# Kernel tuning notes

Measured on AMD Instinct MI355X. Metric: run time of the kernel, lower is better.

## Reference

```python
import jax, jax.numpy as jnp
import numpy as np

N, NFEAT, NHID, NCLASS = 16384, 512, 64, 40
K, ALPHA = 10, 0.1


def setup_inputs() -> dict:
    key = jax.random.key(0)
    k1, k2, k3, k4 = jax.random.split(key, 4)
    x = jax.random.normal(k1, (N, NFEAT), dtype=jnp.float32)
    # dense (row-normalized) propagation matrix, as a PPR transition matrix
    adj = jax.random.uniform(k2, (N, N), dtype=jnp.float32)
    adj = adj / jnp.sum(adj, axis=1, keepdims=True)
    # kaiming-like scaled weights (bias=False in the module)
    W1 = jax.random.normal(k3, (NFEAT, NHID), dtype=jnp.float32) * np.sqrt(2.0 / NFEAT)
    W2 = jax.random.normal(k4, (NHID, NCLASS), dtype=jnp.float32) * np.sqrt(2.0 / NHID)
    return {"x": x, "adj": adj, "W1": W1, "W2": W2}


def reference(x, adj, W1, W2):
    # eval mode: dropout is identity
    h0 = jax.nn.relu(x @ W1)                      # [N, NHID]
    # K-step personalized-PageRank propagation
    def step(x_cl, _):
        return (1.0 - ALPHA) * (adj @ x_cl) + ALPHA * h0, None
    x_cl, _ = jax.lax.scan(step, h0, None, length=K)
    h = x_cl @ W2                                 # [N, NCLASS]
    return jax.nn.log_softmax(h, axis=-1), x_cl
```

## Files before the change

### kernel.cpp

```cpp
#include <hip/hip_runtime.h>

#define NN 16384
#define NF 512
#define NH 64
#define NC 40
#define KSTEPS 10
#define KSPLIT 8
#define BM 32
#define PKH 8
#define ASCALE 8192.0f

typedef __attribute__((ext_vector_type(8))) short short8;
typedef __attribute__((ext_vector_type(4))) float f32x4;
typedef __attribute__((ext_vector_type(2))) long longx2;

__device__ __forceinline__ unsigned short f2bf(float f) {
    unsigned int u = __float_as_uint(f);
    u += 0x7FFFu + ((u >> 16) & 1u);
    return (unsigned short)(u >> 16);
}
__device__ __forceinline__ float bf2f(unsigned short h) {
    return __uint_as_float((unsigned int)h << 16);
}
__device__ __forceinline__ short8 cvt8(float4 f0, float4 f1) {
    short8 r;
    r[0] = (short)f2bf(f0.x); r[1] = (short)f2bf(f0.y);
    r[2] = (short)f2bf(f0.z); r[3] = (short)f2bf(f0.w);
    r[4] = (short)f2bf(f1.x); r[5] = (short)f2bf(f1.y);
    r[6] = (short)f2bf(f1.z); r[7] = (short)f2bf(f1.w);
    return r;
}
__device__ __forceinline__ int pack4fp8(float x0, float x1, float x2, float x3) {
    int r = __builtin_amdgcn_cvt_pk_fp8_f32(x0, x1, 0, false);
    return __builtin_amdgcn_cvt_pk_fp8_f32(x2, x3, r, true);
}
__device__ __forceinline__ longx2 ntload_l2(const unsigned char* p) {
    return __builtin_nontemporal_load((const longx2*)p);
}

__global__ __launch_bounds__(256) void h0_kernel(const float* __restrict__ x,
                                                 const float* __restrict__ W1,
                                                 unsigned short* __restrict__ h0T) {
    const int t  = threadIdx.x;
    const int rl = t & 63;
    const int w  = t >> 6;
    const size_t r = (size_t)blockIdx.x * 64 + rl;
    const float* xr = x + r * NF;

    float acc[16];
#pragma unroll
    for (int j = 0; j < 16; ++j) acc[j] = 0.f;

    for (int k = 0; k < NF; k += 4) {
        float4 xv = *(const float4*)&xr[k];
#pragma unroll
        for (int i = 0; i < 4; ++i) {
            float xs = (i == 0) ? xv.x : (i == 1) ? xv.y : (i == 2) ? xv.z : xv.w;
            const float* wr = W1 + (size_t)(k + i) * NH + w * 16;
#pragma unroll
            for (int j = 0; j < 16; ++j) acc[j] = fmaf(xs, wr[j], acc[j]);
        }
    }
#pragma unroll
    for (int j = 0; j < 16; ++j)
        h0T[(size_t)(w * 16 + j) * NN + r] = f2bf(fmaxf(acc[j], 0.f));
}

__global__ __launch_bounds__(256) void cvtfp8_kernel(const unsigned short* __restrict__ in,
                                                     unsigned char* __restrict__ out,
                                                     long n8) {
    long i = (long)blockIdx.x * blockDim.x + threadIdx.x;
    if (i >= n8) return;
    short8 v = *(const short8*)&in[i * 8];
    int2 o;
    o.x = pack4fp8(bf2f((unsigned short)v[0]), bf2f((unsigned short)v[1]),
                   bf2f((unsigned short)v[2]), bf2f((unsigned short)v[3]));
    o.y = pack4fp8(bf2f((unsigned short)v[4]), bf2f((unsigned short)v[5]),
                   bf2f((unsigned short)v[6]), bf2f((unsigned short)v[7]));
    *(int2*)&out[i * 8] = o;
}

__device__ __forceinline__ void finish_block(float buf[KSPLIT][BM][65],
                                             const f32x4 (&acc)[2][4],
                                             int t, int l, int w, int row0,
                                             const unsigned short* __restrict__ h0T,
                                             unsigned short* __restrict__ xnT,
                                             unsigned char* __restrict__ xnT8) {
    const int fr = l & 15;
    const int fg = l >> 4;
#pragma unroll
    for (int mi = 0; mi < 2; ++mi)
#pragma unroll
        for (int ni = 0; ni < 4; ++ni)
#pragma unroll
            for (int r = 0; r < 4; ++r)
                buf[w][16 * mi + 4 * fg + r][16 * ni + fr] = acc[mi][ni][r];
    __syncthreads();

    const int col = t >> 3;
    const int rb  = 4 * (t & 7);
    float s0 = 0.f, s1 = 0.f, s2 = 0.f, s3 = 0.f;
#pragma unroll
    for (int ww = 0; ww < KSPLIT; ++ww) {
        s0 += buf[ww][rb + 0][col];
        s1 += buf[ww][rb + 1][col];
        s2 += buf[ww][rb + 2][col];
        s3 += buf[ww][rb + 3][col];
    }
    const size_t base = (size_t)col * NN + row0 + rb;
    ushort4 h4 = *(const ushort4*)&h0T[base];
    float v0 = 0.9f * s0 + 0.1f * bf2f(h4.x);
    float v1 = 0.9f * s1 + 0.1f * bf2f(h4.y);
    float v2 = 0.9f * s2 + 0.1f * bf2f(h4.z);
    float v3 = 0.9f * s3 + 0.1f * bf2f(h4.w);
    ushort4 o;
    o.x = f2bf(v0); o.y = f2bf(v1); o.z = f2bf(v2); o.w = f2bf(v3);
    *(ushort4*)&xnT[base] = o;
    if (xnT8)
        *(int*)&xnT8[base] = pack4fp8(v0, v1, v2, v3);
}

__global__ __launch_bounds__(512, 2) void step0_kernel(
        const float* __restrict__ adj,
        unsigned char* __restrict__ adjT8,
        const unsigned short* __restrict__ xT,
        const unsigned short* __restrict__ h0T,
        unsigned short* __restrict__ xnT,
        unsigned char* __restrict__ xnT8) {
    __shared__ float buf[KSPLIT][BM][65];

    const int t    = threadIdx.x;
    const int l    = t & 63;
    const int w    = t >> 6;
    const int fr   = l & 15;
    const int fg   = l >> 4;
    const int row0 = blockIdx.x * BM;

    const size_t a0 = (size_t)(row0 + fr) * NN;
    const size_t a1 = a0 + (size_t)16 * NN;
    const long   kbase = (long)w * (NN / KSPLIT) + 8 * fg;

    f32x4 acc[2][4];
#pragma unroll
    for (int mi = 0; mi < 2; ++mi)
#pragma unroll
        for (int ni = 0; ni < 4; ++ni) acc[mi][ni] = (f32x4){0.f, 0.f, 0.f, 0.f};

    for (int kk = 0; kk < NN / KSPLIT; kk += 64) {
        const long kb      = kbase + kk;
        const size_t ktile = (size_t)w * 32 + (kk >> 6);
        short8 a[2][2], b[4][2];

#pragma unroll
        for (int mi = 0; mi < 2; ++mi) {
            const size_t ab = (mi ? a1 : a0);
            int4 pk;
#pragma unroll
            for (int h = 0; h < 2; ++h) {
                float4 f0 = *(const float4*)&adj[ab + kb + 32 * h];
                float4 f1 = *(const float4*)&adj[ab + kb + 32 * h + 4];
                a[mi][h] = cvt8(f0, f1);
                int plo = pack4fp8(ASCALE * f0.x, ASCALE * f0.y,
                                   ASCALE * f0.z, ASCALE * f0.w);
                int phi = pack4fp8(ASCALE * f1.x, ASCALE * f1.y,
                                   ASCALE * f1.z, ASCALE * f1.w);
                if (h == 0) { pk.x = plo; pk.y = phi; }
                else        { pk.z = plo; pk.w = phi; }
            }
            const size_t st = ((size_t)(2 * blockIdx.x + mi) * 256 + ktile) * 1024
                              + (size_t)l * 16;
            *(int4*)&adjT8[st] = pk;
        }
#pragma unroll
        for (int ni = 0; ni < 4; ++ni)
#pragma unroll
            for (int h = 0; h < 2; ++h)
                b[ni][h] = *(const short8*)&xT[(size_t)(16 * ni + fr) * NN + kb + 32 * h];

#pragma unroll
        for (int mi = 0; mi < 2; ++mi)
#pragma unroll
            for (int ni = 0; ni < 4; ++ni)
#pragma unroll
                for (int h = 0; h < 2; ++h)
                    acc[mi][ni] = __builtin_amdgcn_mfma_f32_16x16x32_bf16(
                        a[mi][h], b[ni][h], acc[mi][ni], 0, 0, 0);
    }
    finish_block(buf, acc, t, l, w, row0, h0T, xnT, xnT8);
}

__global__ __launch_bounds__(512, 4) void stept_kernel(
        const unsigned char* __restrict__ adjT8,
        const unsigned char* __restrict__ xT8,
        float* __restrict__ P) {
    __shared__ unsigned char BLF[2][4096];

    const int t  = threadIdx.x;
    const int l  = t & 63;
    const int w  = t >> 6;
    const int fr = l & 15;
    const int fg = l >> 4;
    const int kh = blockIdx.x & 7;
    const int rt = blockIdx.x >> 3;
    const int kb0 = kh * (NN / PKH);

    const unsigned char* At0 = adjT8
        + (((size_t)(rt * 16 + 2 * w) * 256) + (size_t)(kh * 32)) * 1024 + (size_t)l * 16;
    const unsigned char* At1 = At0 + (size_t)256 * 1024;

    const size_t bsrc = (size_t)(16 * (w >> 1) + fr) * NN + 32 * (w & 1) + 8 * fg;
    unsigned char* st0 = &BLF[0][t * 8];
    unsigned char* st1 = &BLF[1][t * 8];

    f32x4 acc[2][4];
#pragma unroll
    for (int mi = 0; mi < 2; ++mi)
#pragma unroll
        for (int ni = 0; ni < 4; ++ni) acc[mi][ni] = (f32x4){0.f, 0.f, 0.f, 0.f};

    *(long*)st0 = *(const long*)&xT8[bsrc + kb0];
    __syncthreads();

#pragma unroll 2
    for (int i = 0; i < 32; ++i) {
        const unsigned char* rdbuf = (i & 1) ? BLF[1] : BLF[0];
        unsigned char* stbuf = (i & 1) ? st0 : st1;
        if (i + 1 < 32)
            *(long*)stbuf = *(const long*)&xT8[bsrc + kb0 + (i + 1) * 64];

        longx2 a0 = ntload_l2(At0);
        longx2 a1 = ntload_l2(At1);
        At0 += 1024;
        At1 += 1024;

        long b[4][2];
#pragma unroll
        for (int ni = 0; ni < 4; ++ni)
#pragma unroll
            for (int h = 0; h < 2; ++h)
                b[ni][h] = *(const long*)&rdbuf[(size_t)((ni * 2 + h) * 64 + l) * 8];

#pragma unroll
        for (int ni = 0; ni < 4; ++ni) {
            acc[0][ni] = __builtin_amdgcn_mfma_f32_16x16x32_fp8_fp8(a0.x, b[ni][0], acc[0][ni], 0, 0, 0);
            acc[0][ni] = __builtin_amdgcn_mfma_f32_16x16x32_fp8_fp8(a0.y, b[ni][1], acc[0][ni], 0, 0, 0);
            acc[1][ni] = __builtin_amdgcn_mfma_f32_16x16x32_fp8_fp8(a1.x, b[ni][0], acc[1][ni], 0, 0, 0);
            acc[1][ni] = __builtin_amdgcn_mfma_f32_16x16x32_fp8_fp8(a1.y, b[ni][1], acc[1][ni], 0, 0, 0);
        }
        __syncthreads();
    }

    const size_t rowbase = (size_t)rt * 256 + w * 32;
#pragma unroll
    for (int mi = 0; mi < 2; ++mi)
#pragma unroll
        for (int ni = 0; ni < 4; ++ni)
#pragma unroll
            for (int r = 0; r < 4; ++r)
                P[(((size_t)kh * NN) + rowbase + mi * 16 + 4 * fg + r) * 64 + 16 * ni + fr]
                    = acc[mi][ni][r];
}

__global__ __launch_bounds__(256) void combine_kernel(
        const float* __restrict__ P,
        const unsigned short* __restrict__ h0T,
        unsigned short* __restrict__ xnT,
        unsigned char* __restrict__ xnT8) {
    __shared__ float LS[64][65];
    const int t  = threadIdx.x;
    const int r0 = blockIdx.x * 64;

    {
        const int rl = t >> 2;
        const int c0 = (t & 3) * 16;
        f32x4 s[4];
#pragma unroll
        for (int q = 0; q < 4; ++q) s[q] = (f32x4){0.f, 0.f, 0.f, 0.f};
#pragma unroll
        for (int kh = 0; kh < PKH; ++kh) {
            const float* p = &P[(((size_t)kh * NN) + r0 + rl) * 64 + c0];
#pragma unroll
            for (int q = 0; q < 4; ++q) s[q] += *(const f32x4*)&p[q * 4];
        }
#pragma unroll
        for (int q = 0; q < 4; ++q)
            *(f32x4*)&LS[rl][c0 + q * 4] = s[q];
    }
    __syncthreads();

    {
        const int c  = t >> 2;
        const int rs = (t & 3) * 16;
        float vf[16];
        short8 v[2];
#pragma unroll
        for (int j = 0; j < 16; ++j) {
            vf[j] = (0.9f / ASCALE) * LS[rs + j][c]
                  + 0.1f * bf2f(h0T[(size_t)c * NN + r0 + rs + j]);
            v[j >> 3][j & 7] = (short)f2bf(vf[j]);
        }
        *(short8*)&xnT[(size_t)c * NN + r0 + rs]     = v[0];
        *(short8*)&xnT[(size_t)c * NN + r0 + rs + 8] = v[1];
        int4 pk;
        pk.x = pack4fp8(vf[0],  vf[1],  vf[2],  vf[3]);
        pk.y = pack4fp8(vf[4],  vf[5],  vf[6],  vf[7]);
        pk.z = pack4fp8(vf[8],  vf[9],  vf[10], vf[11]);
        pk.w = pack4fp8(vf[12], vf[13], vf[14], vf[15]);
        *(int4*)&xnT8[(size_t)c * NN + r0 + rs] = pk;
    }
}

__global__ __launch_bounds__(512, 4) void stepf_kernel(
        const float* __restrict__ adj,
        const unsigned short* __restrict__ xT,
        const unsigned short* __restrict__ h0T,
        unsigned short* __restrict__ xnT) {
    __shared__ float buf[KSPLIT][BM][65];

    const int t    = threadIdx.x;
    const int l    = t & 63;
    const int w    = t >> 6;
    const int fr   = l & 15;
    const int row0 = blockIdx.x * BM;

    const size_t a0 = (size_t)(row0 + fr) * NN;
    const size_t a1 = a0 + (size_t)16 * NN;
    const long   kbase = (long)w * (NN / KSPLIT) + 8 * (l >> 4);

    f32x4 acc[2][4];
#pragma unroll
    for (int mi = 0; mi < 2; ++mi)
#pragma unroll
        for (int ni = 0; ni < 4; ++ni) acc[mi][ni] = (f32x4){0.f, 0.f, 0.f, 0.f};

    for (int kk = 0; kk < NN / KSPLIT; kk += 64) {
        const long kb = kbase + kk;
        short8 a[2][2], b[4][2];
#pragma unroll
        for (int mi = 0; mi < 2; ++mi) {
            const size_t ab = (mi ? a1 : a0);
#pragma unroll
            for (int h = 0; h < 2; ++h) {
                float4 f0 = *(const float4*)&adj[ab + kb + 32 * h];
                float4 f1 = *(const float4*)&adj[ab + kb + 32 * h + 4];
                a[mi][h] = cvt8(f0, f1);
            }
        }
#pragma unroll
        for (int ni = 0; ni < 4; ++ni)
#pragma unroll
            for (int h = 0; h < 2; ++h)
                b[ni][h] = *(const short8*)&xT[(size_t)(16 * ni + fr) * NN + kb + 32 * h];
#pragma unroll
        for (int mi = 0; mi < 2; ++mi)
#pragma unroll
            for (int ni = 0; ni < 4; ++ni)
#pragma unroll
                for (int h = 0; h < 2; ++h)
                    acc[mi][ni] = __builtin_amdgcn_mfma_f32_16x16x32_bf16(
                        a[mi][h], b[ni][h], acc[mi][ni], 0, 0, 0);
    }
    finish_block(buf, acc, t, l, w, row0, h0T, xnT, nullptr);
}

__global__ __launch_bounds__(256) void final_kernel(const unsigned short* __restrict__ xT,
                                                    const float* __restrict__ W2,
                                                    float* __restrict__ out_ls,
                                                    float* __restrict__ out_x) {
    __shared__ float LS[64][65];
    const int t  = threadIdx.x;
    const int rl = t & 63;
    const int w  = t >> 6;
    const int r0 = blockIdx.x * 64;

#pragma unroll
    for (int j = 0; j < 16; ++j) {
        int c = w * 16 + j;
        LS[c][rl] = bf2f(xT[(size_t)c * NN + r0 + rl]);
    }
    __syncthreads();

#pragma unroll
    for (int k2 = 0; k2 < 16; ++k2) {
        int idx = k2 * 256 + t;
        int row = idx >> 6, col = idx & 63;
        out_x[(size_t)(r0 + row) * NH + col] = LS[col][row];
    }

    float acc[NC];
    if (t < 64) {
#pragma unroll
        for (int j = 0; j < NC; ++j) acc[j] = 0.f;
        for (int c = 0; c < NH; ++c) {
            float xv = LS[c][t];
            const float* wr = W2 + (size_t)c * NC;
#pragma unroll
            for (int j = 0; j < NC; ++j) acc[j] = fmaf(xv, wr[j], acc[j]);
        }
        float m = acc[0];
#pragma unroll
        for (int j = 1; j < NC; ++j) m = fmaxf(m, acc[j]);
        float s = 0.f;
#pragma unroll
        for (int j = 0; j < NC; ++j) s += expf(acc[j] - m);
        float lg = m + logf(s);
#pragma unroll
        for (int j = 0; j < NC; ++j) acc[j] -= lg;
    }
    __syncthreads();
    if (t < 64) {
#pragma unroll
        for (int j = 0; j < NC; ++j) LS[t][j] = acc[j];
    }
    __syncthreads();
    for (int i = t; i < 64 * NC; i += 256) {
        int row = i / NC, j = i - row * NC;
        out_ls[(size_t)r0 * NC + i] = LS[row][j];
    }
}

extern "C" void kernel_launch(void* const* d_in, const int* in_sizes, int n_in,
                              void* d_out, int out_size, void* d_ws, size_t ws_size,
                              hipStream_t stream) {
    const float* x   = (const float*)d_in[0];
    const float* adj = (const float*)d_in[1];
    const float* W1  = (const float*)d_in[2];
    const float* W2  = (const float*)d_in[3];

    float* out_ls = (float*)d_out;
    float* out_x  = out_ls + (size_t)NN * NC;

    const size_t xbytes  = (size_t)NN * NH * sizeof(unsigned short);
    const size_t x8bytes = (size_t)NN * NH;
    char* ws = (char*)d_ws;

    unsigned short *h0T, *xa, *xb;
    unsigned char  *h0T8, *xa8, *xb8;
    size_t used;
    if (ws_size >= 3 * xbytes + 3 * x8bytes) {
        h0T  = (unsigned short*)ws;
        xa   = (unsigned short*)(ws + xbytes);
        xb   = (unsigned short*)(ws + 2 * xbytes);
        h0T8 = (unsigned char*)(ws + 3 * xbytes);
        xa8  = h0T8 + x8bytes;
        xb8  = xa8 + x8bytes;
        used = 3 * xbytes + 3 * x8bytes;
    } else {
        xa  = (unsigned short*)ws;
        xb  = xa + (size_t)NN * NH;
        h0T = (unsigned short*)out_ls;
        h0T8 = xa8 = xb8 = nullptr;
        used = 2 * xbytes;
    }
    used = (used + 255) & ~(size_t)255;

    const size_t pbytes    = (size_t)PKH * NN * NH * sizeof(float);
    const size_t adj8bytes = (size_t)NN * NN;

    float* P = nullptr;
    unsigned char* adjT8 = nullptr;
    if (h0T8 && ws_size >= used + pbytes + adj8bytes) {
        P     = (float*)(ws + used);
        adjT8 = (unsigned char*)(ws + used + pbytes);
    }

    h0_kernel<<<NN / 64, 256, 0, stream>>>(x, W1, h0T);

    unsigned short* cur  = h0T;
    unsigned short* nxt  = xa;
    unsigned char*  cur8 = h0T8;
    unsigned char*  nxt8 = xa8;

    if (adjT8)
        cvtfp8_kernel<<<(NN * NH / 8 + 255) / 256, 256, 0, stream>>>(
            h0T, h0T8, (long)NN * NH / 8);

    for (int s = 0; s < KSTEPS; ++s) {
        if (adjT8) {
            if (s == 0) {
                step0_kernel<<<NN / BM, 512, 0, stream>>>(adj, adjT8, cur, h0T, nxt, nxt8);
            } else {
                stept_kernel<<<(NN / 256) * PKH, 512, 0, stream>>>(adjT8, cur8, P);
                combine_kernel<<<NN / 64, 256, 0, stream>>>(P, h0T, nxt, nxt8);
            }
        } else {
            stepf_kernel<<<NN / BM, 512, 0, stream>>>(adj, cur, h0T, nxt);
        }
        unsigned short* ts  = (cur == h0T) ? xb : cur;
        unsigned char*  ts8 = (cur8 == h0T8) ? xb8 : cur8;
        cur = nxt;  nxt = ts;
        cur8 = nxt8; nxt8 = ts8;
    }

    final_kernel<<<NN / 64, 256, 0, stream>>>(cur, W2, out_ls, out_x);
}
```

Before: 1.048 ms.

## Restructure step0 into split-K tiles via LDS, store partials as bf16

The first propagation step is rewritten to use 16-row tiles split eight ways along K, like the later fp8 steps. Each block stages the fp32 adjacency rows into LDS as bf16, then packs them into the transposed fp8 layout. Partial sums go to a shared buffer reduced by combine_kernel, which now takes a scale argument. The partial buffer P drops from fp32 to bf16 to halve its write and read traffic. The separate h0 fp8 conversion kernel is removed, at the cost of extra bf16 rounding in the partials.

```diff
diff --git a/kernel.cpp b/kernel.cpp
--- a/kernel.cpp
+++ b/kernel.cpp
@@ -66,133 +66,108 @@
         h0T[(size_t)(w * 16 + j) * NN + r] = f2bf(fmaxf(acc[j], 0.f));
 }
 
-__global__ __launch_bounds__(256) void cvtfp8_kernel(const unsigned short* __restrict__ in,
-                                                     unsigned char* __restrict__ out,
-                                                     long n8) {
-    long i = (long)blockIdx.x * blockDim.x + threadIdx.x;
-    if (i >= n8) return;
-    short8 v = *(const short8*)&in[i * 8];
-    int2 o;
-    o.x = pack4fp8(bf2f((unsigned short)v[0]), bf2f((unsigned short)v[1]),
-                   bf2f((unsigned short)v[2]), bf2f((unsigned short)v[3]));
-    o.y = pack4fp8(bf2f((unsigned short)v[4]), bf2f((unsigned short)v[5]),
-                   bf2f((unsigned short)v[6]), bf2f((unsigned short)v[7]));
-    *(int2*)&out[i * 8] = o;
-}
-
-__device__ __forceinline__ void finish_block(float buf[KSPLIT][BM][65],
-                                             const f32x4 (&acc)[2][4],
-                                             int t, int l, int w, int row0,
-                                             const unsigned short* __restrict__ h0T,
-                                             unsigned short* __restrict__ xnT,
-                                             unsigned char* __restrict__ xnT8) {
-    const int fr = l & 15;
-    const int fg = l >> 4;
-#pragma unroll
-    for (int mi = 0; mi < 2; ++mi)
-#pragma unroll
-        for (int ni = 0; ni < 4; ++ni)
-#pragma unroll
-            for (int r = 0; r < 4; ++r)
-                buf[w][16 * mi + 4 * fg + r][16 * ni + fr] = acc[mi][ni][r];
-    __syncthreads();
-
-    const int col = t >> 3;
-    const int rb  = 4 * (t & 7);
-    float s0 = 0.f, s1 = 0.f, s2 = 0.f, s3 = 0.f;
-#pragma unroll
-    for (int ww = 0; ww < KSPLIT; ++ww) {
-        s0 += buf[ww][rb + 0][col];
-        s1 += buf[ww][rb + 1][col];
-        s2 += buf[ww][rb + 2][col];
-        s3 += buf[ww][rb + 3][col];
-    }
-    const size_t base = (size_t)col * NN + row0 + rb;
-    ushort4 h4 = *(const ushort4*)&h0T[base];
-    float v0 = 0.9f * s0 + 0.1f * bf2f(h4.x);
-    float v1 = 0.9f * s1 + 0.1f * bf2f(h4.y);
-    float v2 = 0.9f * s2 + 0.1f * bf2f(h4.z);
-    float v3 = 0.9f * s3 + 0.1f * bf2f(h4.w);
-    ushort4 o;
-    o.x = f2bf(v0); o.y = f2bf(v1); o.z = f2bf(v2); o.w = f2bf(v3);
-    *(ushort4*)&xnT[base] = o;
-    if (xnT8)
-        *(int*)&xnT8[base] = pack4fp8(v0, v1, v2, v3);
-}
-
-__global__ __launch_bounds__(512, 2) void step0_kernel(
+__global__ __launch_bounds__(512, 4) void step0_kernel(
         const float* __restrict__ adj,
         unsigned char* __restrict__ adjT8,
         const unsigned short* __restrict__ xT,
-        const unsigned short* __restrict__ h0T,
-        unsigned short* __restrict__ xnT,
-        unsigned char* __restrict__ xnT8) {
-    __shared__ float buf[KSPLIT][BM][65];
-
-    const int t    = threadIdx.x;
-    const int l    = t & 63;
-    const int w    = t >> 6;
-    const int fr   = l & 15;
-    const int fg   = l >> 4;
-    const int row0 = blockIdx.x * BM;
-
-    const size_t a0 = (size_t)(row0 + fr) * NN;
-    const size_t a1 = a0 + (size_t)16 * NN;
-    const long   kbase = (long)w * (NN / KSPLIT) + 8 * fg;
-
-    f32x4 acc[2][4];
-#pragma unroll
-    for (int mi = 0; mi < 2; ++mi)
-#pragma unroll
-        for (int ni = 0; ni < 4; ++ni) acc[mi][ni] = (f32x4){0.f, 0.f, 0.f, 0.f};
-
-    for (int kk = 0; kk < NN / KSPLIT; kk += 64) {
-        const long kb      = kbase + kk;
-        const size_t ktile = (size_t)w * 32 + (kk >> 6);
-        short8 a[2][2], b[4][2];
-
-#pragma unroll
-        for (int mi = 0; mi < 2; ++mi) {
-            const size_t ab = (mi ? a1 : a0);
+        unsigned short* __restrict__ P) {
+    __shared__ __align__(16) unsigned char SMEM[33280];
+    unsigned short (*AT)[1032] = (unsigned short (*)[1032])SMEM;
+    float (*FB)[16][65] = (float (*)[16][65])SMEM;
+
+    const int t  = threadIdx.x;
+    const int l  = t & 63;
+    const int w  = t >> 6;
+    const int fr = l & 15;
+    const int fg = l >> 4;
+    const int kh = blockIdx.x & 7;
+    const int mt = blockIdx.x >> 3;
+    const int r0 = mt * 16;
+    const long ks0 = (long)kh * (NN / PKH);
+
+    f32x4 acc[4];
+#pragma unroll
+    for (int ni = 0; ni < 4; ++ni) acc[ni] = (f32x4){0.f, 0.f, 0.f, 0.f};
+
+#pragma unroll
+    for (int chunk = 0; chunk < 2; ++chunk) {
+        const long kc0 = ks0 + chunk * 1024;
+        __syncthreads();
+#pragma unroll
+        for (int rr = 0; rr < 2; ++rr) {
+            const int row = 2 * w + rr;
+            const float* src = &adj[(size_t)(r0 + row) * NN + kc0];
+#pragma unroll
+            for (int q = 0; q < 4; ++q) {
+                float4 v = *(const float4*)&src[q * 256 + l * 4];
+                ushort4 o;
+                o.x = f2bf(v.x); o.y = f2bf(v.y); o.z = f2bf(v.z); o.w = f2bf(v.w);
+                *(ushort4*)&AT[row][q * 256 + l * 4] = o;
+            }
+        }
+        __syncthreads();
+#pragma unroll
+        for (int tt = 0; tt < 2; ++tt) {
+            const int tl = 2 * w + tt;
+            short8 a0 = *(const short8*)&AT[fr][tl * 64 + 8 * fg];
+            short8 a1 = *(const short8*)&AT[fr][tl * 64 + 32 + 8 * fg];
+
             int4 pk;
-#pragma unroll
-            for (int h = 0; h < 2; ++h) {
-                float4 f0 = *(const float4*)&adj[ab + kb + 32 * h];
-                float4 f1 = *(const float4*)&adj[ab + kb + 32 * h + 4];
-                a[mi][h] = cvt8(f0, f1);
-                int plo = pack4fp8(ASCALE * f0.x, ASCALE * f0.y,
-                                   ASCALE * f0.z, ASCALE * f0.w);
-                int phi = pack4fp8(ASCALE * f1.x, ASCALE * f1.y,
-                                   ASCALE * f1.z, ASCALE * f1.w);
-                if (h == 0) { pk.x = plo; pk.y = phi; }
-                else        { pk.z = plo; pk.w = phi; }
-            }
-            const size_t st = ((size_t)(2 * blockIdx.x + mi) * 256 + ktile) * 1024
+            pk.x = pack4fp8(ASCALE * bf2f((unsigned short)a0[0]),
+                            ASCALE * bf2f((unsigned short)a0[1]),
+                            ASCALE * bf2f((unsigned short)a0[2]),
+                            ASCALE * bf2f((unsigned short)a0[3]));
+            pk.y = pack4fp8(ASCALE * bf2f((unsigned short)a0[4]),
+                            ASCALE * bf2f((unsigned short)a0[5]),
+                            ASCALE * bf2f((unsigned short)a0[6]),
+                            ASCALE * bf2f((unsigned short)a0[7]));
+            pk.z = pack4fp8(ASCALE * bf2f((unsigned short)a1[0]),
+                            ASCALE * bf2f((unsigned short)a1[1]),
+                            ASCALE * bf2f((unsigned short)a1[2]),
+                            ASCALE * bf2f((unsigned short)a1[3]));
+            pk.w = pack4fp8(ASCALE * bf2f((unsigned short)a1[4]),
+                            ASCALE * bf2f((unsigned short)a1[5]),
+                            ASCALE * bf2f((unsigned short)a1[6]),
+                            ASCALE * bf2f((unsigned short)a1[7]));
+            const size_t st = ((size_t)mt * 256 + kh * 32 + chunk * 16 + tl) * 1024
                               + (size_t)l * 16;
             *(int4*)&adjT8[st] = pk;
-        }
-#pragma unroll
-        for (int ni = 0; ni < 4; ++ni)
-#pragma unroll
-            for (int h = 0; h < 2; ++h)
-                b[ni][h] = *(const short8*)&xT[(size_t)(16 * ni + fr) * NN + kb + 32 * h];
-
-#pragma unroll
-        for (int mi = 0; mi < 2; ++mi)
-#pragma unroll
-            for (int ni = 0; ni < 4; ++ni)
-#pragma unroll
-                for (int h = 0; h < 2; ++h)
-                    acc[mi][ni] = __builtin_amdgcn_mfma_f32_16x16x32_bf16(
-                        a[mi][h], b[ni][h], acc[mi][ni], 0, 0, 0);
-    }
-    finish_block(buf, acc, t, l, w, row0, h0T, xnT, xnT8);
+
+            const long kb = kc0 + tl * 64 + 8 * fg;
+#pragma unroll
+            for (int ni = 0; ni < 4; ++ni) {
+                short8 b0 = *(const short8*)&xT[(size_t)(16 * ni + fr) * NN + kb];
+                short8 b1 = *(const short8*)&xT[(size_t)(16 * ni + fr) * NN + kb + 32];
+                acc[ni] = __builtin_amdgcn_mfma_f32_16x16x32_bf16(a0, b0, acc[ni], 0, 0, 0);
+                acc[ni] = __builtin_amdgcn_mfma_f32_16x16x32_bf16(a1, b1, acc[ni], 0, 0, 0);
+            }
+        }
+    }
+
+    __syncthreads();
+#pragma unroll
+    for (int ni = 0; ni < 4; ++ni)
+#pragma unroll
+        for (int r = 0; r < 4; ++r)
+            FB[w][4 * fg + r][16 * ni + fr] = acc[ni][r];
+    __syncthreads();
+
+    const int col = t & 63;
+    const int rw2 = t >> 6;
+#pragma unroll
+    for (int rr = 0; rr < 2; ++rr) {
+        const int row = 2 * rw2 + rr;
+        float s = 0.f;
+#pragma unroll
+        for (int ww = 0; ww < 8; ++ww) s += FB[ww][row][col];
+        P[((size_t)kh * NN + r0 + row) * 64 + col] = f2bf(s);
+    }
 }
 
 __global__ __launch_bounds__(512, 4) void stept_kernel(
         const unsigned char* __restrict__ adjT8,
         const unsigned char* __restrict__ xT8,
-        float* __restrict__ P) {
+        unsigned short* __restrict__ P) {
     __shared__ unsigned char BLF[2][4096];
 
     const int t  = threadIdx.x;
@@ -258,14 +233,15 @@
 #pragma unroll
             for (int r = 0; r < 4; ++r)
                 P[(((size_t)kh * NN) + rowbase + mi * 16 + 4 * fg + r) * 64 + 16 * ni + fr]
-                    = acc[mi][ni][r];
+                    = f2bf(acc[mi][ni][r]);
 }
 
 __global__ __launch_bounds__(256) void combine_kernel(
-        const float* __restrict__ P,
+        const unsigned short* __restrict__ P,
         const unsigned short* __restrict__ h0T,
         unsigned short* __restrict__ xnT,
-        unsigned char* __restrict__ xnT8) {
+        unsigned char* __restrict__ xnT8,
+        float scale) {
     __shared__ float LS[64][65];
     const int t  = threadIdx.x;
     const int r0 = blockIdx.x * 64;
@@ -273,18 +249,22 @@
     {
         const int rl = t >> 2;
         const int c0 = (t & 3) * 16;
-        f32x4 s[4];
-#pragma unroll
-        for (int q = 0; q < 4; ++q) s[q] = (f32x4){0.f, 0.f, 0.f, 0.f};
+        float s[16];
+#pragma unroll
+        for (int j = 0; j < 16; ++j) s[j] = 0.f;
 #pragma unroll
         for (int kh = 0; kh < PKH; ++kh) {
-            const float* p = &P[(((size_t)kh * NN) + r0 + rl) * 64 + c0];
-#pragma unroll
-            for (int q = 0; q < 4; ++q) s[q] += *(const f32x4*)&p[q * 4];
-        }
-#pragma unroll
-        for (int q = 0; q < 4; ++q)
-            *(f32x4*)&LS[rl][c0 + q * 4] = s[q];
+            const unsigned short* p = &P[(((size_t)kh * NN) + r0 + rl) * 64 + c0];
+            short8 v0 = *(const short8*)&p[0];
+            short8 v1 = *(const short8*)&p[8];
+#pragma unroll
+            for (int j = 0; j < 8; ++j) {
+                s[j]     += bf2f((unsigned short)v0[j]);
+                s[8 + j] += bf2f((unsigned short)v1[j]);
+            }
+        }
+#pragma unroll
+        for (int j = 0; j < 16; ++j) LS[rl][c0 + j] = s[j];
     }
     __syncthreads();
 
@@ -295,7 +275,7 @@
         short8 v[2];
 #pragma unroll
         for (int j = 0; j < 16; ++j) {
-            vf[j] = (0.9f / ASCALE) * LS[rs + j][c]
+            vf[j] = scale * LS[rs + j][c]
                   + 0.1f * bf2f(h0T[(size_t)c * NN + r0 + rs + j]);
             v[j >> 3][j & 7] = (short)f2bf(vf[j]);
         }
@@ -310,6 +290,42 @@
     }
 }
 
+__device__ __forceinline__ void finish_blockf(float buf[KSPLIT][BM][65],
+                                              const f32x4 (&acc)[2][4],
+                                              int t, int l, int w, int row0,
+                                              const unsigned short* __restrict__ h0T,
+                                              unsigned short* __restrict__ xnT) {
+    const int fr = l & 15;
+    const int fg = l >> 4;
+#pragma unroll
+    for (int mi = 0; mi < 2; ++mi)
+#pragma unroll
+        for (int ni = 0; ni < 4; ++ni)
+#pragma unroll
+            for (int r = 0; r < 4; ++r)
+                buf[w][16 * mi + 4 * fg + r][16 * ni + fr] = acc[mi][ni][r];
+    __syncthreads();
+
+    const int col = t >> 3;
+    const int rb  = 4 * (t & 7);
+    float s0 = 0.f, s1 = 0.f, s2 = 0.f, s3 = 0.f;
+#pragma unroll
+    for (int ww = 0; ww < KSPLIT; ++ww) {
+        s0 += buf[ww][rb + 0][col];
+        s1 += buf[ww][rb + 1][col];
+        s2 += buf[ww][rb + 2][col];
+        s3 += buf[ww][rb + 3][col];
+    }
+    const size_t base = (size_t)col * NN + row0 + rb;
+    ushort4 h4 = *(const ushort4*)&h0T[base];
+    ushort4 o;
+    o.x = f2bf(0.9f * s0 + 0.1f * bf2f(h4.x));
+    o.y = f2bf(0.9f * s1 + 0.1f * bf2f(h4.y));
+    o.z = f2bf(0.9f * s2 + 0.1f * bf2f(h4.z));
+    o.w = f2bf(0.9f * s3 + 0.1f * bf2f(h4.w));
+    *(ushort4*)&xnT[base] = o;
+}
+
 __global__ __launch_bounds__(512, 4) void stepf_kernel(
         const float* __restrict__ adj,
         const unsigned short* __restrict__ xT,
@@ -360,7 +376,7 @@
                     acc[mi][ni] = __builtin_amdgcn_mfma_f32_16x16x32_bf16(
                         a[mi][h], b[ni][h], acc[mi][ni], 0, 0, 0);
     }
-    finish_block(buf, acc, t, l, w, row0, h0T, xnT, nullptr);
+    finish_blockf(buf, acc, t, l, w, row0, h0T, xnT);
 }
 
 __global__ __launch_bounds__(256) void final_kernel(const unsigned short* __restrict__ xT,
@@ -435,32 +451,31 @@
     char* ws = (char*)d_ws;
 
     unsigned short *h0T, *xa, *xb;
-    unsigned char  *h0T8, *xa8, *xb8;
+    unsigned char  *xa8, *xb8;
     size_t used;
-    if (ws_size >= 3 * xbytes + 3 * x8bytes) {
-        h0T  = (unsigned short*)ws;
-        xa   = (unsigned short*)(ws + xbytes);
-        xb   = (unsigned short*)(ws + 2 * xbytes);
-        h0T8 = (unsigned char*)(ws + 3 * xbytes);
-        xa8  = h0T8 + x8bytes;
-        xb8  = xa8 + x8bytes;
-        used = 3 * xbytes + 3 * x8bytes;
+    if (ws_size >= 3 * xbytes + 2 * x8bytes) {
+        h0T = (unsigned short*)ws;
+        xa  = (unsigned short*)(ws + xbytes);
+        xb  = (unsigned short*)(ws + 2 * xbytes);
+        xa8 = (unsigned char*)(ws + 3 * xbytes);
+        xb8 = xa8 + x8bytes;
+        used = 3 * xbytes + 2 * x8bytes;
     } else {
         xa  = (unsigned short*)ws;
         xb  = xa + (size_t)NN * NH;
         h0T = (unsigned short*)out_ls;
-        h0T8 = xa8 = xb8 = nullptr;
+        xa8 = xb8 = nullptr;
         used = 2 * xbytes;
     }
     used = (used + 255) & ~(size_t)255;
 
-    const size_t pbytes    = (size_t)PKH * NN * NH * sizeof(float);
+    const size_t pbytes    = (size_t)PKH * NN * NH * sizeof(unsigned short);
     const size_t adj8bytes = (size_t)NN * NN;
 
-    float* P = nullptr;
+    unsigned short* P = nullptr;
     unsigned char* adjT8 = nullptr;
-    if (h0T8 && ws_size >= used + pbytes + adj8bytes) {
-        P     = (float*)(ws + used);
+    if (xa8 && ws_size >= used + pbytes + adj8bytes) {
+        P     = (unsigned short*)(ws + used);
         adjT8 = (unsigned char*)(ws + used + pbytes);
     }
 
@@ -468,27 +483,23 @@
 
     unsigned short* cur  = h0T;
     unsigned short* nxt  = xa;
-    unsigned char*  cur8 = h0T8;
+    unsigned char*  cur8 = nullptr;
     unsigned char*  nxt8 = xa8;
-
-    if (adjT8)
-        cvtfp8_kernel<<<(NN * NH / 8 + 255) / 256, 256, 0, stream>>>(
-            h0T, h0T8, (long)NN * NH / 8);
 
     for (int s = 0; s < KSTEPS; ++s) {
         if (adjT8) {
-            if (s == 0) {
-                step0_kernel<<<NN / BM, 512, 0, stream>>>(adj, adjT8, cur, h0T, nxt, nxt8);
-            } else {
+            if (s == 0)
+                step0_kernel<<<(NN / 16) * PKH / 8 * 8, 512, 0, stream>>>(adj, adjT8, cur, P);
+            else
                 stept_kernel<<<(NN / 256) * PKH, 512, 0, stream>>>(adjT8, cur8, P);
-                combine_kernel<<<NN / 64, 256, 0, stream>>>(P, h0T, nxt, nxt8);
-            }
+            combine_kernel<<<NN / 64, 256, 0, stream>>>(
+                P, h0T, nxt, nxt8, (s == 0) ? 0.9f : 0.9f / ASCALE);
         } else {
             stepf_kernel<<<NN / BM, 512, 0, stream>>>(adj, cur, h0T, nxt);
         }
         unsigned short* ts  = (cur == h0T) ? xb : cur;
-        unsigned char*  ts8 = (cur8 == h0T8) ? xb8 : cur8;
-        cur = nxt;  nxt = ts;
+        unsigned char*  ts8 = (cur8 == nullptr) ? xb8 : cur8;
+        cur = nxt;   nxt = ts;
         cur8 = nxt8; nxt8 = ts8;
     }
 
```

Result: slower. 1.071 ms (+2.2%).
